# Optimization experiments

Hardware: AMD Instinct MI355X
Metric: run time of the kernel (lower is better)

## Reference

```python
import jax, jax.numpy as jnp
import numpy as np

KAPPA = 10000.0
B_CONST = 0.5


def pe_matrix(L, dim):
    # pe[j,i] = sin(j/kappa^(i/dim)) for even i, cos(j/kappa^((i-1)/dim)) for odd i
    j = jnp.arange(L, dtype=jnp.float32)[:, None]
    i = jnp.arange(dim, dtype=jnp.float32)[None, :]
    even = (jnp.arange(dim) % 2 == 0)[None, :]
    expo = jnp.where(even, i, i - 1.0) / dim
    ang = j / (KAPPA ** expo)
    return jnp.where(even, jnp.sin(ang), jnp.cos(ang))  # [L, dim]


def setup_inputs() -> dict:
    key = jax.random.key(0)
    ks = jax.random.split(key, 6)
    B, N, L, d, n = 4, 8, 1024, 256, 3
    theta = jax.random.normal(ks[0], (B, N, L, d), dtype=jnp.float32)
    xi = jax.random.normal(ks[1], (B, N, L, n), dtype=jnp.float32)
    edge_attr = jax.random.normal(ks[2], (B, L, N * (N - 1) * 2), dtype=jnp.float32)
    s = 1.0 / np.sqrt(d)
    Wq = jax.random.normal(ks[3], (d, d), dtype=jnp.float32) * s
    Wk = jax.random.normal(ks[4], (d, d), dtype=jnp.float32) * s
    Wv = jax.random.normal(ks[5], (d, d), dtype=jnp.float32) * s
    return {"theta": theta, "xi": xi, "edge_attr": edge_attr, "Wq": Wq, "Wk": Wk, "Wv": Wv}


def reference(theta, xi, edge_attr, Wq, Wk, Wv):
    B, N, L, d = theta.shape
    n = xi.shape[-1]
    # positional encoding (dropout in eval mode = identity)
    theta = theta + pe_matrix(L, d)
    xi = xi + pe_matrix(L, n)
    edge_attr = edge_attr + pe_matrix(L, N * (N - 1) * 2)[None]

    causal = jnp.triu(jnp.ones((L, L), dtype=bool), 1)  # True above diagonal
    neg_inf = jnp.float32(-jnp.inf)

    # feature path: standard causal scaled-dot-product attention
    q = jnp.einsum('bnld,ed->bnle', theta, Wq)
    k = jnp.einsum('bnld,ed->bnle', theta, Wk)
    v = jnp.einsum('bnld,ed->bnle', theta, Wv)
    scores = jnp.einsum('bnqd,bnkd->bnqk', q, k) / jnp.sqrt(jnp.float32(d))
    scores = jnp.where(causal, neg_inf, scores)
    h_out = jnp.einsum('bnqk,bnkd->bnqd', jax.nn.softmax(scores, axis=-1), v)

    # equivariant path: pairwise squared-distance attention
    D = xi[:, :, :, None, :] - xi[:, :, None, :, :]  # [B,N,L,L,n]
    sq = jnp.sum(D * D, axis=-1)                     # [B,N,L,L]
    sq = jnp.where(causal, neg_inf, sq)
    beta = jax.nn.softmax(sq, axis=-1)
    mbeta = beta * (1.0 - jnp.eye(L, dtype=beta.dtype))  # zero the diagonal
    second = B_CONST * jnp.einsum('bnqk,bnkc->bnqc', mbeta, xi)
    third = B_CONST * jnp.sum(mbeta, axis=-1, keepdims=True) * xi
    x_out = xi + second - third

    return h_out, x_out, edge_attr
```

## Files before the change

### kernel.cpp

```cpp
#include <hip/hip_runtime.h>
#include <math.h>

#define L    1024
#define D    256
#define NCH  3
#define HEADS 32
#define EDIM 112
#define BATCH 4

typedef __bf16 bf8_t __attribute__((ext_vector_type(8)));
typedef float  f4_t  __attribute__((ext_vector_type(4)));

typedef __attribute__((address_space(1))) const void GVC;
typedef __attribute__((address_space(3))) void LDSV;

__device__ inline unsigned short f2bf(float x) {
    unsigned u = __float_as_uint(x);
    u += 0x7FFFu + ((u >> 16) & 1u);
    return (unsigned short)(u >> 16);
}
__device__ inline float bf2f(unsigned short h) {
    return __uint_as_float(((unsigned)h) << 16);
}

__global__ void prep_kernel(const float* __restrict__ edge, const float* __restrict__ xi,
                            const float* __restrict__ Wq, const float* __restrict__ Wk,
                            const float* __restrict__ Wv,
                            float* __restrict__ pe_d, float* __restrict__ eout,
                            float* __restrict__ xsb, unsigned short* __restrict__ whb)
{
    int idx = blockIdx.x * blockDim.x + threadIdx.x;
    if (idx < L * D) {
        int l = idx >> 8, i = idx & (D - 1);
        float expo = (float)(i & ~1) * (1.0f / (float)D);
        float ang = (float)l * __powf(10000.0f, -expo);
        pe_d[idx] = (i & 1) ? cosf(ang) : sinf(ang);
    } else if (idx < L * D + BATCH * L * EDIM) {
        int j = idx - L * D;
        int i = j % EDIM;
        int l = (j / EDIM) % L;
        float expo = (float)(i & ~1) * (1.0f / (float)EDIM);
        float ang = (float)l * __powf(10000.0f, -expo);
        eout[j] = edge[j] + ((i & 1) ? cosf(ang) : sinf(ang));
    } else if (idx < L * D + BATCH * L * EDIM + HEADS * L * NCH) {
        int j = idx - (L * D + BATCH * L * EDIM);
        int c = j % 3;
        int l = (j / 3) & (L - 1);
        float ang = (c == 2) ? (float)l * 0.0021544347f : (float)l;
        float pe = (c == 1) ? cosf(ang) : sinf(ang);
        xsb[j] = xi[j] + pe;
    } else {
        int j = idx - (L * D + BATCH * L * EDIM + HEADS * L * NCH);
        if (j < 3 * 8192) {
            int wsel = j >> 13;
            int t = j & 8191;
            int g = t >> 9, u = (t >> 4) & 31, rr = t & 15;
            const float* W = (wsel == 0) ? Wq : (wsel == 1) ? Wk : Wv;
            const float4* s = reinterpret_cast<const float4*>(&W[(size_t)(g * 16 + rr) * D + u * 8]);
            float4 a = s[0], b = s[1];
            float x[8] = {a.x, a.y, a.z, a.w, b.x, b.y, b.z, b.w};
            union { unsigned short us[8]; float4 f4; } hv;
            #pragma unroll
            for (int q = 0; q < 8; q++) hv.us[q] = f2bf(x[q]);
            *reinterpret_cast<float4*>(&whb[(size_t)wsel * 65536 + g * 4096 + u * 128 + rr * 8]) = hv.f4;
        }
    }
}

__global__ __launch_bounds__(512) void qkv_mfma(
    const float* __restrict__ theta, const float* __restrict__ pe_d,
    const unsigned short* __restrict__ whb,
    unsigned short* __restrict__ qh, unsigned short* __restrict__ ql,
    unsigned short* __restrict__ kh, unsigned short* __restrict__ vt)
{
    __shared__ __align__(16) unsigned short XsH[2][4096];
    __shared__ __align__(16) unsigned short XsL[2][4096];
    __shared__ __align__(16) unsigned short Ws[2][8192];

    int tid = threadIdx.x;
    int w = tid >> 6, lane = tid & 63;
    int quad = lane >> 4, l16 = lane & 15;
    int eh = w & 1;
    int xq = w >> 1;

    int b = blockIdx.x;
    int xcd = b & 7, r = b >> 3;
    int wsel = r % 3;
    int panel = (r / 3) * 8 + xcd;
    int rowBase = panel * 128;
    const unsigned short* wsrc = whb + (size_t)wsel * 65536;

    int sr = tid >> 2;
    int ks8 = (tid & 3) * 8;
    int cg = sr >> 4, cr = sr & 15, cu = tid & 3;
    int xoff = cg * 512 + cu * 128 + cr * 8;

    const float* tp_base = &theta[(size_t)(rowBase + sr) * D + ks8];
    const float* pp_base = &pe_d[(size_t)((rowBase + sr) & (L - 1)) * D + ks8];

    f4_t acc[16];
    #pragma unroll
    for (int i = 0; i < 16; i++) acc[i] = (f4_t){0.f, 0.f, 0.f, 0.f};

    auto stageW = [&](int kt, int buf) {
        #pragma unroll
        for (int j = 0; j < 2; j++) {
            int g = w * 2 + j;
            __builtin_amdgcn_global_load_lds(
                (GVC*)(wsrc + (size_t)g * 4096 + kt * 512 + lane * 8),
                (LDSV*)(Ws[buf] + g * 512), 16, 0, 0);
        }
    };
    auto loadX = [&](int kt, float* xv) {
        const float* tp = tp_base + kt * 32;
        const float* pp = pp_base + kt * 32;
        float4 t0 = reinterpret_cast<const float4*>(tp)[0];
        float4 t1 = reinterpret_cast<const float4*>(tp)[1];
        float4 p0 = reinterpret_cast<const float4*>(pp)[0];
        float4 p1 = reinterpret_cast<const float4*>(pp)[1];
        xv[0] = t0.x + p0.x; xv[1] = t0.y + p0.y; xv[2] = t0.z + p0.z; xv[3] = t0.w + p0.w;
        xv[4] = t1.x + p1.x; xv[5] = t1.y + p1.y; xv[6] = t1.z + p1.z; xv[7] = t1.w + p1.w;
    };
    auto convX = [&](const float* xv, int buf) {
        union { unsigned short us[8]; float4 f4; } h, lo;
        #pragma unroll
        for (int e = 0; e < 8; e++) {
            unsigned short hh = f2bf(xv[e]);
            h.us[e] = hh;
            lo.us[e] = f2bf(xv[e] - bf2f(hh));
        }
        *reinterpret_cast<float4*>(&XsH[buf][xoff]) = h.f4;
        *reinterpret_cast<float4*>(&XsL[buf][xoff]) = lo.f4;
    };

    {
        float xv[8];
        loadX(0, xv);
        convX(xv, 0);
        stageW(0, 0);
    }
    __syncthreads();

    #define FR(buf2d, g16) (*reinterpret_cast<const bf8_t*>(&(buf2d)[(g16) * 512 + quad * 128 + l16 * 8]))

    for (int kt = 0; kt < 8; kt++) {
        int buf = kt & 1;

        float xn[8];
        if (kt < 7) {
            stageW(kt + 1, buf ^ 1);
            loadX(kt + 1, xn);
        }
        __builtin_amdgcn_sched_barrier(0);

        bf8_t bxh[2], bxl[2];
        #pragma unroll
        for (int nx = 0; nx < 2; nx++) {
            bxh[nx] = FR(XsH[buf], xq * 2 + nx);
            bxl[nx] = FR(XsL[buf], xq * 2 + nx);
        }

        if (wsel < 2) {
            #pragma unroll
            for (int ne = 0; ne < 8; ne++) {
                bf8_t aw = FR(Ws[buf], eh * 8 + ne);
                #pragma unroll
                for (int nx = 0; nx < 2; nx++) {
                    acc[ne * 2 + nx] = __builtin_amdgcn_mfma_f32_16x16x32_bf16(aw, bxh[nx], acc[ne * 2 + nx], 0, 0, 0);
                    acc[ne * 2 + nx] = __builtin_amdgcn_mfma_f32_16x16x32_bf16(aw, bxl[nx], acc[ne * 2 + nx], 0, 0, 0);
                }
            }
        } else {
            #pragma unroll
            for (int ne = 0; ne < 8; ne++) {
                bf8_t bw = FR(Ws[buf], eh * 8 + ne);
                #pragma unroll
                for (int mx = 0; mx < 2; mx++) {
                    acc[mx * 8 + ne] = __builtin_amdgcn_mfma_f32_16x16x32_bf16(bxh[mx], bw, acc[mx * 8 + ne], 0, 0, 0);
                    acc[mx * 8 + ne] = __builtin_amdgcn_mfma_f32_16x16x32_bf16(bxl[mx], bw, acc[mx * 8 + ne], 0, 0, 0);
                }
            }
        }

        if (kt < 7) convX(xn, buf ^ 1);
        __syncthreads();
    }
    #undef FR

    if (wsel < 2) {
        float scale = (wsel == 0) ? 0.0625f : 1.0f;
        #pragma unroll
        for (int ne = 0; ne < 8; ne++) {
            #pragma unroll
            for (int nx = 0; nx < 2; nx++) {
                int e0 = eh * 128 + ne * 16 + quad * 4;
                size_t row = rowBase + xq * 32 + nx * 16 + l16;
                union { unsigned short us[4]; unsigned long long u; } ph, pl;
                #pragma unroll
                for (int rr = 0; rr < 4; rr++) {
                    float x = acc[ne * 2 + nx][rr] * scale;
                    unsigned short h = f2bf(x);
                    ph.us[rr] = h;
                    pl.us[rr] = f2bf(x - bf2f(h));
                }
                if (wsel == 0) {
                    *reinterpret_cast<unsigned long long*>(&qh[row * D + e0]) = ph.u;
                    *reinterpret_cast<unsigned long long*>(&ql[row * D + e0]) = pl.u;
                } else {
                    int e0s = e0 ^ ((l16 & 7) << 3);
                    *reinterpret_cast<unsigned long long*>(&kh[row * D + e0s]) = ph.u;
                }
            }
        }
    } else {
        #pragma unroll
        for (int mx = 0; mx < 2; mx++) {
            #pragma unroll
            for (int ne = 0; ne < 8; ne++) {
                int row0 = rowBase + xq * 32 + mx * 16 + quad * 4;
                int e = eh * 128 + ne * 16 + l16;
                int head = row0 >> 10, kb = (row0 & 1023) >> 5, kk = row0 & 31;
                union { unsigned short us[4]; unsigned long long u; } pk;
                #pragma unroll
                for (int rr = 0; rr < 4; rr++) pk.us[rr] = f2bf(acc[mx * 8 + ne][rr]);
                int us_sw = (e * 32 + kk) ^ (((e >> 1) & 3) << 3);
                *reinterpret_cast<unsigned long long*>(
                    &vt[((size_t)(head * 32 + kb)) * 8192 + us_sw]) = pk.u;
            }
        }
    }
}

__device__ __forceinline__ void stage_tile(
    const unsigned short* kht, const unsigned short* vtt,
    unsigned short* Ks, unsigned short* Vs, int kt, int buf, int w, int lane)
{
    #pragma unroll
    for (int i = 0; i < 2; i++) {
        int ch = w * 2 + i;
        __builtin_amdgcn_global_load_lds(
            (GVC*)(kht + (size_t)kt * 8192 + ch * 512 + lane * 8),
            (LDSV*)(Ks + buf * 8192 + ch * 512), 16, 0, 0);
        __builtin_amdgcn_global_load_lds(
            (GVC*)(vtt + (size_t)kt * 8192 + ch * 512 + lane * 8),
            (LDSV*)(Vs + buf * 8192 + ch * 512), 16, 0, 0);
    }
}

__global__ __launch_bounds__(512) void attn_v7(
    const unsigned short* __restrict__ qh, const unsigned short* __restrict__ ql,
    const unsigned short* __restrict__ kh, const unsigned short* __restrict__ vt,
    float* __restrict__ hout)
{
    __shared__ __align__(16) unsigned short Ks[2 * 8192];
    __shared__ __align__(16) unsigned short Vs[2 * 8192];
    __shared__ __align__(16) unsigned short Pb[8][16 * 40];
    __shared__ unsigned short lds_pad[4200];

    int tid = threadIdx.x;
    int w = tid >> 6, lane = tid & 63;
    int quad = lane >> 4, l16 = lane & 15;
    int b = blockIdx.x;
    int head = ((b & 7) << 2) + (b >> 6);
    int s = (b >> 3) & 7;
    int u = (w < 4) ? (4 * s + w) : (63 - 4 * s - (w - 4));
    int Ts = 32 - 2 * s;
    int lim = u >> 1;
    size_t hb = (size_t)head * (L * D);
    const unsigned short* kht = kh + hb;
    const unsigned short* vtt = vt + (size_t)head * (32 * 8192);
    unsigned short* Pw = Pb[w];

    if (hout == nullptr) lds_pad[tid] = 1;

    int q_g = u * 16 + l16;

    f4_t qfh[8], qfl[8];
    {
        const unsigned short* ph = qh + hb + (size_t)q_g * D + quad * 8;
        const unsigned short* pl = ql + hb + (size_t)q_g * D + quad * 8;
        #pragma unroll
        for (int c = 0; c < 8; c++) {
            qfh[c] = *reinterpret_cast<const f4_t*>(ph + c * 32);
            qfl[c] = *reinterpret_cast<const f4_t*>(pl + c * 32);
        }
    }
    #pragma unroll
    for (int c = 0; c < 8; c++) {
        asm volatile("" : "+v"(qfh[c]));
        asm volatile("" : "+v"(qfl[c]));
    }

    stage_tile(kht, vtt, Ks, Vs, 0, 0, w, lane);

    f4_t acc[16];
    #pragma unroll
    for (int i = 0; i < 16; i++) acc[i] = (f4_t){0.f, 0.f, 0.f, 0.f};
    float mrun = -1e30f, lrun = 0.f;

    int xm = (l16 & 7) << 3;
    int vq = (quad * 8) ^ (((l16 >> 1) & 3) << 3);

    asm volatile("s_waitcnt vmcnt(0)" ::: "memory");
    __syncthreads();

    #pragma unroll 1
    for (int kt = 0; kt < Ts; kt++) {
        if (kt + 1 < Ts)
            stage_tile(kht, vtt, Ks, Vs, kt + 1, (kt + 1) & 1, w, lane);

        if (kt <= lim) {
            const unsigned short* Kb = Ks + (kt & 1) * 8192;
            const unsigned short* Vb = Vs + (kt & 1) * 8192;
            int kBase = kt * 32;

            bf8_t kf0[8], kf1[8];
            #pragma unroll
            for (int c = 0; c < 8; c++) {
                int col = (quad * 8 + c * 32) ^ xm;
                kf0[c] = *reinterpret_cast<const bf8_t*>(&Kb[l16 * 256 + col]);
                kf1[c] = *reinterpret_cast<const bf8_t*>(&Kb[(16 + l16) * 256 + col]);
            }
            const unsigned short* vpb = Vb + l16 * 32 + vq;
            bf8_t vfA[8];
            #pragma unroll
            for (int dt = 0; dt < 8; dt++)
                vfA[dt] = *reinterpret_cast<const bf8_t*>(vpb + dt * 512);

            f4_t s0a = (f4_t){0.f,0.f,0.f,0.f}, s0b = (f4_t){0.f,0.f,0.f,0.f};
            f4_t s1a = (f4_t){0.f,0.f,0.f,0.f}, s1b = (f4_t){0.f,0.f,0.f,0.f};
            #pragma unroll
            for (int c = 0; c < 8; c += 2) {
                s0a = __builtin_amdgcn_mfma_f32_16x16x32_bf16(kf0[c],     __builtin_bit_cast(bf8_t, qfh[c]),     s0a, 0, 0, 0);
                s0b = __builtin_amdgcn_mfma_f32_16x16x32_bf16(kf0[c + 1], __builtin_bit_cast(bf8_t, qfh[c + 1]), s0b, 0, 0, 0);
                s0a = __builtin_amdgcn_mfma_f32_16x16x32_bf16(kf0[c],     __builtin_bit_cast(bf8_t, qfl[c]),     s0a, 0, 0, 0);
                s0b = __builtin_amdgcn_mfma_f32_16x16x32_bf16(kf0[c + 1], __builtin_bit_cast(bf8_t, qfl[c + 1]), s0b, 0, 0, 0);
            }
            #pragma unroll
            for (int c = 0; c < 8; c += 2) {
                s1a = __builtin_amdgcn_mfma_f32_16x16x32_bf16(kf1[c],     __builtin_bit_cast(bf8_t, qfh[c]),     s1a, 0, 0, 0);
                s1b = __builtin_amdgcn_mfma_f32_16x16x32_bf16(kf1[c + 1], __builtin_bit_cast(bf8_t, qfh[c + 1]), s1b, 0, 0, 0);
                s1a = __builtin_amdgcn_mfma_f32_16x16x32_bf16(kf1[c],     __builtin_bit_cast(bf8_t, qfl[c]),     s1a, 0, 0, 0);
                s1b = __builtin_amdgcn_mfma_f32_16x16x32_bf16(kf1[c + 1], __builtin_bit_cast(bf8_t, qfl[c + 1]), s1b, 0, 0, 0);
            }
            f4_t sc[2];
            sc[0] = s0a + s0b;
            sc[1] = s1a + s1b;

            float pv[2][4];
            float tm = -1e30f;
            #pragma unroll
            for (int t = 0; t < 2; t++)
                #pragma unroll
                for (int rr = 0; rr < 4; rr++) {
                    int key = kBase + t * 16 + quad * 4 + rr;
                    float sv = (key <= q_g) ? sc[t][rr] : -1e30f;
                    sc[t][rr] = sv;
                    tm = fmaxf(tm, sv);
                }
            tm = fmaxf(tm, __shfl_xor(tm, 16));
            tm = fmaxf(tm, __shfl_xor(tm, 32));
            bool grow = __any(tm > mrun);
            float mnew = fmaxf(mrun, tm);
            float alpha = grow ? __expf(mrun - mnew) : 1.0f;
            mrun = mnew;
            float ts = 0.f;
            #pragma unroll
            for (int t = 0; t < 2; t++)
                #pragma unroll
                for (int rr = 0; rr < 4; rr++) {
                    float p = __expf(sc[t][rr] - mnew);
                    pv[t][rr] = p;
                    ts += p;
                }
            ts += __shfl_xor(ts, 16);
            ts += __shfl_xor(ts, 32);
            lrun = lrun * alpha + ts;

            #pragma unroll
            for (int t = 0; t < 2; t++) {
                union { unsigned short us[4]; unsigned long long uu; } pk;
                #pragma unroll
                for (int rr = 0; rr < 4; rr++) pk.us[rr] = f2bf(pv[t][rr]);
                *reinterpret_cast<unsigned long long*>(&Pw[l16 * 40 + t * 16 + quad * 4]) = pk.uu;
            }
            bf8_t vfB[8];
            #pragma unroll
            for (int dt = 0; dt < 8; dt++)
                vfB[dt] = *reinterpret_cast<const bf8_t*>(vpb + (8 + dt) * 512);
            if (grow) {
                #pragma unroll
                for (int dt = 0; dt < 16; dt++) acc[dt] *= alpha;
            }
            asm volatile("s_waitcnt lgkmcnt(0)" ::: "memory");
            bf8_t pf = *reinterpret_cast<const bf8_t*>(&Pw[l16 * 40 + quad * 8]);
            #pragma unroll
            for (int dt = 0; dt < 8; dt++)
                acc[dt] = __builtin_amdgcn_mfma_f32_16x16x32_bf16(vfA[dt], pf, acc[dt], 0, 0, 0);
            #pragma unroll
            for (int dt = 0; dt < 8; dt++)
                acc[8 + dt] = __builtin_amdgcn_mfma_f32_16x16x32_bf16(vfB[dt], pf, acc[8 + dt], 0, 0, 0);
        }

        asm volatile("s_waitcnt vmcnt(0)" ::: "memory");
        __syncthreads();
    }

    float inv = 1.f / lrun;
    float* dst = hout + hb + (size_t)q_g * D + quad * 4;
    #pragma unroll
    for (int dt = 0; dt < 16; dt++) {
        float4 o = {acc[dt][0] * inv, acc[dt][1] * inv,
                    acc[dt][2] * inv, acc[dt][3] * inv};
        *reinterpret_cast<float4*>(dst + dt * 16) = o;
    }
}

__global__ __launch_bounds__(256) void equiv_kernel(
    const float* __restrict__ xsb, float* __restrict__ xout)
{
    __shared__ float xs[L * NCH];
    int head = blockIdx.y;
    int tid = threadIdx.x;
    const float4* src = reinterpret_cast<const float4*>(xsb + (size_t)head * L * NCH);
    #pragma unroll
    for (int it = 0; it < 3; it++)
        reinterpret_cast<float4*>(xs)[tid + it * 256] = src[tid + it * 256];
    __syncthreads();

    int w = tid >> 6, lane = tid & 63;
    int q = blockIdx.x * 4 + w;
    float xq0 = xs[q * 3 + 0], xq1 = xs[q * 3 + 1], xq2 = xs[q * 3 + 2];

    float m = 0.f;
    for (int k = lane; k < q; k += 64) {
        float d0 = xq0 - xs[k * 3 + 0];
        float d1 = xq1 - xs[k * 3 + 1];
        float d2 = xq2 - xs[k * 3 + 2];
        m = fmaxf(m, d0 * d0 + d1 * d1 + d2 * d2);
    }
    #pragma unroll
    for (int off = 1; off < 64; off <<= 1) m = fmaxf(m, __shfl_xor(m, off));

    float s0 = 0.f, s1 = 0.f, s2 = 0.f, sn = 0.f;
    for (int k = lane; k < q; k += 64) {
        float d0 = xq0 - xs[k * 3 + 0];
        float d1 = xq1 - xs[k * 3 + 1];
        float d2 = xq2 - xs[k * 3 + 2];
        float wgt = __expf(d0 * d0 + d1 * d1 + d2 * d2 - m);
        sn += wgt;
        s0 += wgt * xs[k * 3 + 0];
        s1 += wgt * xs[k * 3 + 1];
        s2 += wgt * xs[k * 3 + 2];
    }
    #pragma unroll
    for (int off = 1; off < 64; off <<= 1) {
        sn += __shfl_xor(sn, off);
        s0 += __shfl_xor(s0, off);
        s1 += __shfl_xor(s1, off);
        s2 += __shfl_xor(s2, off);
    }
    float Z = sn + __expf(-m);
    float inv = 0.5f / Z;
    if (lane == 0) {
        size_t ob = (size_t)head * L * NCH + (size_t)q * NCH;
        xout[ob + 0] = xq0 + inv * (s0 - sn * xq0);
        xout[ob + 1] = xq1 + inv * (s1 - sn * xq1);
        xout[ob + 2] = xq2 + inv * (s2 - sn * xq2);
    }
}

extern "C" void kernel_launch(void* const* d_in, const int* in_sizes, int n_in,
                              void* d_out, int out_size, void* d_ws, size_t ws_size,
                              hipStream_t stream)
{
    (void)in_sizes; (void)n_in; (void)out_size; (void)ws_size;
    const float* theta = (const float*)d_in[0];
    const float* xi    = (const float*)d_in[1];
    const float* edge  = (const float*)d_in[2];
    const float* Wq    = (const float*)d_in[3];
    const float* Wk    = (const float*)d_in[4];
    const float* Wv    = (const float*)d_in[5];

    float* out  = (float*)d_out;
    float* hout = out;
    float* xout = out + 8388608;
    float* eout = out + 8388608 + 98304;

    const size_t NE = 8388608;
    unsigned short* base = (unsigned short*)d_ws;
    unsigned short* qh  = base;
    unsigned short* ql  = base + NE;
    unsigned short* kh  = base + 2 * NE;
    unsigned short* vt  = base + 3 * NE;
    unsigned short* whb = base + 4 * NE;
    float* pe_d = (float*)(base + 4 * NE + 196608);
    float* xsb  = pe_d + L * D;

    prep_kernel<<<3296, 256, 0, stream>>>(edge, xi, Wq, Wk, Wv, pe_d, eout, xsb, whb);
    equiv_kernel<<<dim3(L / 4, HEADS), 256, 0, stream>>>(xsb, xout);
    qkv_mfma<<<768, 512, 0, stream>>>(theta, pe_d, whb, qh, ql, kh, vt);
    attn_v7<<<256, 512, 0, stream>>>(qh, ql, kh, vt, hout);
}
```

Baseline: 230.6 us.

## Deepen LDS pipelines to four stages and keep activations in registers

```diff
diff --git a/kernel.cpp b/kernel.cpp
--- a/kernel.cpp
+++ b/kernel.cpp
@@ -73,9 +73,7 @@
     unsigned short* __restrict__ qh, unsigned short* __restrict__ ql,
     unsigned short* __restrict__ kh, unsigned short* __restrict__ vt)
 {
-    __shared__ __align__(16) unsigned short XsH[2][4096];
-    __shared__ __align__(16) unsigned short XsL[2][4096];
-    __shared__ __align__(16) unsigned short Ws[2][8192];
+    __shared__ __align__(16) unsigned short Ws[4][8192];
 
     int tid = threadIdx.x;
     int w = tid >> 6, lane = tid & 63;
@@ -90,18 +88,6 @@
     int rowBase = panel * 128;
     const unsigned short* wsrc = whb + (size_t)wsel * 65536;
 
-    int sr = tid >> 2;
-    int ks8 = (tid & 3) * 8;
-    int cg = sr >> 4, cr = sr & 15, cu = tid & 3;
-    int xoff = cg * 512 + cu * 128 + cr * 8;
-
-    const float* tp_base = &theta[(size_t)(rowBase + sr) * D + ks8];
-    const float* pp_base = &pe_d[(size_t)((rowBase + sr) & (L - 1)) * D + ks8];
-
-    f4_t acc[16];
-    #pragma unroll
-    for (int i = 0; i < 16; i++) acc[i] = (f4_t){0.f, 0.f, 0.f, 0.f};
-
     auto stageW = [&](int kt, int buf) {
         #pragma unroll
         for (int j = 0; j < 2; j++) {
@@ -111,54 +97,58 @@
                 (LDSV*)(Ws[buf] + g * 512), 16, 0, 0);
         }
     };
-    auto loadX = [&](int kt, float* xv) {
-        const float* tp = tp_base + kt * 32;
-        const float* pp = pp_base + kt * 32;
-        float4 t0 = reinterpret_cast<const float4*>(tp)[0];
-        float4 t1 = reinterpret_cast<const float4*>(tp)[1];
-        float4 p0 = reinterpret_cast<const float4*>(pp)[0];
-        float4 p1 = reinterpret_cast<const float4*>(pp)[1];
-        xv[0] = t0.x + p0.x; xv[1] = t0.y + p0.y; xv[2] = t0.z + p0.z; xv[3] = t0.w + p0.w;
-        xv[4] = t1.x + p1.x; xv[5] = t1.y + p1.y; xv[6] = t1.z + p1.z; xv[7] = t1.w + p1.w;
-    };
-    auto convX = [&](const float* xv, int buf) {
-        union { unsigned short us[8]; float4 f4; } h, lo;
-        #pragma unroll
-        for (int e = 0; e < 8; e++) {
-            unsigned short hh = f2bf(xv[e]);
-            h.us[e] = hh;
-            lo.us[e] = f2bf(xv[e] - bf2f(hh));
-        }
-        *reinterpret_cast<float4*>(&XsH[buf][xoff]) = h.f4;
-        *reinterpret_cast<float4*>(&XsL[buf][xoff]) = lo.f4;
-    };
-
-    {
-        float xv[8];
-        loadX(0, xv);
-        convX(xv, 0);
-        stageW(0, 0);
-    }
-    __syncthreads();
+
+    stageW(0, 0);
+    stageW(1, 1);
+    stageW(2, 2);
+
+    f4_t xh[2][8], xl[2][8];
+    #pragma unroll
+    for (int nx = 0; nx < 2; nx++) {
+        int row = rowBase + xq * 32 + nx * 16 + l16;
+        const float* tp = &theta[(size_t)row * D + quad * 8];
+        const float* pp = &pe_d[(size_t)(row & (L - 1)) * D + quad * 8];
+        #pragma unroll
+        for (int kt = 0; kt < 8; kt++) {
+            float4 t0 = reinterpret_cast<const float4*>(tp + kt * 32)[0];
+            float4 t1 = reinterpret_cast<const float4*>(tp + kt * 32 + 4)[0];
+            float4 p0 = reinterpret_cast<const float4*>(pp + kt * 32)[0];
+            float4 p1 = reinterpret_cast<const float4*>(pp + kt * 32 + 4)[0];
+            float xv[8] = {t0.x + p0.x, t0.y + p0.y, t0.z + p0.z, t0.w + p0.w,
+                           t1.x + p1.x, t1.y + p1.y, t1.z + p1.z, t1.w + p1.w};
+            union { unsigned short us[8]; f4_t f; } hu, lu;
+            #pragma unroll
+            for (int e = 0; e < 8; e++) {
+                unsigned short hh = f2bf(xv[e]);
+                hu.us[e] = hh;
+                lu.us[e] = f2bf(xv[e] - bf2f(hh));
+            }
+            xh[nx][kt] = hu.f;
+            xl[nx][kt] = lu.f;
+        }
+    }
+    #pragma unroll
+    for (int nx = 0; nx < 2; nx++)
+        #pragma unroll
+        for (int kt = 0; kt < 8; kt++) {
+            asm volatile("" : "+v"(xh[nx][kt]));
+            asm volatile("" : "+v"(xl[nx][kt]));
+        }
+
+    f4_t acc[16];
+    #pragma unroll
+    for (int i = 0; i < 16; i++) acc[i] = (f4_t){0.f, 0.f, 0.f, 0.f};
 
     #define FR(buf2d, g16) (*reinterpret_cast<const bf8_t*>(&(buf2d)[(g16) * 512 + quad * 128 + l16 * 8]))
 
+    #pragma unroll
     for (int kt = 0; kt < 8; kt++) {
-        int buf = kt & 1;
-
-        float xn[8];
-        if (kt < 7) {
-            stageW(kt + 1, buf ^ 1);
-            loadX(kt + 1, xn);
-        }
+        int buf = kt & 3;
+        asm volatile("s_waitcnt vmcnt(4)" ::: "memory");
+        __builtin_amdgcn_s_barrier();
         __builtin_amdgcn_sched_barrier(0);
-
-        bf8_t bxh[2], bxl[2];
-        #pragma unroll
-        for (int nx = 0; nx < 2; nx++) {
-            bxh[nx] = FR(XsH[buf], xq * 2 + nx);
-            bxl[nx] = FR(XsL[buf], xq * 2 + nx);
-        }
+        int nt = (kt + 3 < 8) ? kt + 3 : 7;
+        stageW(nt, (kt + 3) & 3);
 
         if (wsel < 2) {
             #pragma unroll
@@ -166,8 +156,8 @@
                 bf8_t aw = FR(Ws[buf], eh * 8 + ne);
                 #pragma unroll
                 for (int nx = 0; nx < 2; nx++) {
-                    acc[ne * 2 + nx] = __builtin_amdgcn_mfma_f32_16x16x32_bf16(aw, bxh[nx], acc[ne * 2 + nx], 0, 0, 0);
-                    acc[ne * 2 + nx] = __builtin_amdgcn_mfma_f32_16x16x32_bf16(aw, bxl[nx], acc[ne * 2 + nx], 0, 0, 0);
+                    acc[ne * 2 + nx] = __builtin_amdgcn_mfma_f32_16x16x32_bf16(aw, __builtin_bit_cast(bf8_t, xh[nx][kt]), acc[ne * 2 + nx], 0, 0, 0);
+                    acc[ne * 2 + nx] = __builtin_amdgcn_mfma_f32_16x16x32_bf16(aw, __builtin_bit_cast(bf8_t, xl[nx][kt]), acc[ne * 2 + nx], 0, 0, 0);
                 }
             }
         } else {
@@ -176,14 +166,11 @@
                 bf8_t bw = FR(Ws[buf], eh * 8 + ne);
                 #pragma unroll
                 for (int mx = 0; mx < 2; mx++) {
-                    acc[mx * 8 + ne] = __builtin_amdgcn_mfma_f32_16x16x32_bf16(bxh[mx], bw, acc[mx * 8 + ne], 0, 0, 0);
-                    acc[mx * 8 + ne] = __builtin_amdgcn_mfma_f32_16x16x32_bf16(bxl[mx], bw, acc[mx * 8 + ne], 0, 0, 0);
-                }
-            }
-        }
-
-        if (kt < 7) convX(xn, buf ^ 1);
-        __syncthreads();
+                    acc[mx * 8 + ne] = __builtin_amdgcn_mfma_f32_16x16x32_bf16(__builtin_bit_cast(bf8_t, xh[mx][kt]), bw, acc[mx * 8 + ne], 0, 0, 0);
+                    acc[mx * 8 + ne] = __builtin_amdgcn_mfma_f32_16x16x32_bf16(__builtin_bit_cast(bf8_t, xl[mx][kt]), bw, acc[mx * 8 + ne], 0, 0, 0);
+                }
+            }
+        }
     }
     #undef FR
 
@@ -247,15 +234,14 @@
     }
 }
 
-__global__ __launch_bounds__(512) void attn_v7(
+__global__ __launch_bounds__(512) void attn_v9(
     const unsigned short* __restrict__ qh, const unsigned short* __restrict__ ql,
     const unsigned short* __restrict__ kh, const unsigned short* __restrict__ vt,
     float* __restrict__ hout)
 {
-    __shared__ __align__(16) unsigned short Ks[2 * 8192];
-    __shared__ __align__(16) unsigned short Vs[2 * 8192];
+    __shared__ __align__(16) unsigned short Ks[4 * 8192];
+    __shared__ __align__(16) unsigned short Vs[4 * 8192];
     __shared__ __align__(16) unsigned short Pb[8][16 * 40];
-    __shared__ unsigned short lds_pad[4200];
 
     int tid = threadIdx.x;
     int w = tid >> 6, lane = tid & 63;
@@ -271,8 +257,6 @@
     const unsigned short* vtt = vt + (size_t)head * (32 * 8192);
     unsigned short* Pw = Pb[w];
 
-    if (hout == nullptr) lds_pad[tid] = 1;
-
     int q_g = u * 16 + l16;
 
     f4_t qfh[8], qfl[8];
@@ -292,6 +276,8 @@
     }
 
     stage_tile(kht, vtt, Ks, Vs, 0, 0, w, lane);
+    stage_tile(kht, vtt, Ks, Vs, 1, 1, w, lane);
+    stage_tile(kht, vtt, Ks, Vs, 2, 2, w, lane);
 
     f4_t acc[16];
     #pragma unroll
@@ -301,17 +287,17 @@
     int xm = (l16 & 7) << 3;
     int vq = (quad * 8) ^ (((l16 >> 1) & 3) << 3);
 
-    asm volatile("s_waitcnt vmcnt(0)" ::: "memory");
-    __syncthreads();
-
     #pragma unroll 1
     for (int kt = 0; kt < Ts; kt++) {
-        if (kt + 1 < Ts)
-            stage_tile(kht, vtt, Ks, Vs, kt + 1, (kt + 1) & 1, w, lane);
+        asm volatile("s_waitcnt vmcnt(8)" ::: "memory");
+        __builtin_amdgcn_s_barrier();
+        __builtin_amdgcn_sched_barrier(0);
+        int nt = (kt + 3 < Ts) ? kt + 3 : Ts - 1;
+        stage_tile(kht, vtt, Ks, Vs, nt, (kt + 3) & 3, w, lane);
 
         if (kt <= lim) {
-            const unsigned short* Kb = Ks + (kt & 1) * 8192;
-            const unsigned short* Vb = Vs + (kt & 1) * 8192;
+            const unsigned short* Kb = Ks + (kt & 3) * 8192;
+            const unsigned short* Vb = Vs + (kt & 3) * 8192;
             int kBase = kt * 32;
 
             bf8_t kf0[8], kf1[8];
@@ -329,6 +315,7 @@
 
             f4_t s0a = (f4_t){0.f,0.f,0.f,0.f}, s0b = (f4_t){0.f,0.f,0.f,0.f};
             f4_t s1a = (f4_t){0.f,0.f,0.f,0.f}, s1b = (f4_t){0.f,0.f,0.f,0.f};
+            __builtin_amdgcn_s_setprio(1);
             #pragma unroll
             for (int c = 0; c < 8; c += 2) {
                 s0a = __builtin_amdgcn_mfma_f32_16x16x32_bf16(kf0[c],     __builtin_bit_cast(bf8_t, qfh[c]),     s0a, 0, 0, 0);
@@ -343,6 +330,7 @@
                 s1a = __builtin_amdgcn_mfma_f32_16x16x32_bf16(kf1[c],     __builtin_bit_cast(bf8_t, qfl[c]),     s1a, 0, 0, 0);
                 s1b = __builtin_amdgcn_mfma_f32_16x16x32_bf16(kf1[c + 1], __builtin_bit_cast(bf8_t, qfl[c + 1]), s1b, 0, 0, 0);
             }
+            __builtin_amdgcn_s_setprio(0);
             f4_t sc[2];
             sc[0] = s0a + s0b;
             sc[1] = s1a + s1b;
@@ -394,16 +382,15 @@
             }
             asm volatile("s_waitcnt lgkmcnt(0)" ::: "memory");
             bf8_t pf = *reinterpret_cast<const bf8_t*>(&Pw[l16 * 40 + quad * 8]);
+            __builtin_amdgcn_s_setprio(1);
             #pragma unroll
             for (int dt = 0; dt < 8; dt++)
                 acc[dt] = __builtin_amdgcn_mfma_f32_16x16x32_bf16(vfA[dt], pf, acc[dt], 0, 0, 0);
             #pragma unroll
             for (int dt = 0; dt < 8; dt++)
                 acc[8 + dt] = __builtin_amdgcn_mfma_f32_16x16x32_bf16(vfB[dt], pf, acc[8 + dt], 0, 0, 0);
-        }
-
-        asm volatile("s_waitcnt vmcnt(0)" ::: "memory");
-        __syncthreads();
+            __builtin_amdgcn_s_setprio(0);
+        }
     }
 
     float inv = 1.f / lrun;
@@ -500,5 +487,5 @@
     prep_kernel<<<3296, 256, 0, stream>>>(edge, xi, Wq, Wk, Wv, pe_d, eout, xsb, whb);
     equiv_kernel<<<dim3(L / 4, HEADS), 256, 0, stream>>>(xsb, xout);
     qkv_mfma<<<768, 512, 0, stream>>>(theta, pe_d, whb, qh, ql, kh, vt);
-    attn_v7<<<256, 512, 0, stream>>>(qh, ql, kh, vt, hout);
-}
+    attn_v9<<<256, 512, 0, stream>>>(qh, ql, kh, vt, hout);
+}
```

Measured after the change: 273.4 us. +18.5%, slower.

## Process two key tiles per barrier step in causal attention kernel

Applied to the files above, without the earlier changes.

```diff
diff --git a/kernel.cpp b/kernel.cpp
--- a/kernel.cpp
+++ b/kernel.cpp
@@ -231,31 +231,35 @@
     }
 }
 
-__device__ __forceinline__ void stage_tile(
+__device__ __forceinline__ void stage_super(
     const unsigned short* kht, const unsigned short* vtt,
-    unsigned short* Ks, unsigned short* Vs, int kt, int buf, int w, int lane)
+    unsigned short* Ks, unsigned short* Vs, int st, int buf, int w, int lane)
 {
     #pragma unroll
-    for (int i = 0; i < 2; i++) {
-        int ch = w * 2 + i;
-        __builtin_amdgcn_global_load_lds(
-            (GVC*)(kht + (size_t)kt * 8192 + ch * 512 + lane * 8),
-            (LDSV*)(Ks + buf * 8192 + ch * 512), 16, 0, 0);
-        __builtin_amdgcn_global_load_lds(
-            (GVC*)(vtt + (size_t)kt * 8192 + ch * 512 + lane * 8),
-            (LDSV*)(Vs + buf * 8192 + ch * 512), 16, 0, 0);
-    }
-}
-
-__global__ __launch_bounds__(512) void attn_v7(
+    for (int j = 0; j < 2; j++) {
+        int t = st * 2 + j;
+        #pragma unroll
+        for (int i = 0; i < 2; i++) {
+            int ch = w * 2 + i;
+            __builtin_amdgcn_global_load_lds(
+                (GVC*)(kht + (size_t)t * 8192 + ch * 512 + lane * 8),
+                (LDSV*)(Ks + buf * 16384 + j * 8192 + ch * 512), 16, 0, 0);
+            __builtin_amdgcn_global_load_lds(
+                (GVC*)(vtt + (size_t)t * 8192 + ch * 512 + lane * 8),
+                (LDSV*)(Vs + buf * 16384 + j * 8192 + ch * 512), 16, 0, 0);
+        }
+    }
+}
+
+__global__ __launch_bounds__(512) __attribute__((amdgpu_waves_per_eu(2, 2)))
+void attn_v10(
     const unsigned short* __restrict__ qh, const unsigned short* __restrict__ ql,
     const unsigned short* __restrict__ kh, const unsigned short* __restrict__ vt,
     float* __restrict__ hout)
 {
-    __shared__ __align__(16) unsigned short Ks[2 * 8192];
-    __shared__ __align__(16) unsigned short Vs[2 * 8192];
-    __shared__ __align__(16) unsigned short Pb[8][16 * 40];
-    __shared__ unsigned short lds_pad[4200];
+    __shared__ __align__(16) unsigned short Ks[2 * 16384];
+    __shared__ __align__(16) unsigned short Vs[2 * 16384];
+    __shared__ __align__(16) unsigned short Pb[8][2][16 * 40];
 
     int tid = threadIdx.x;
     int w = tid >> 6, lane = tid & 63;
@@ -265,13 +269,13 @@
     int s = (b >> 3) & 7;
     int u = (w < 4) ? (4 * s + w) : (63 - 4 * s - (w - 4));
     int Ts = 32 - 2 * s;
-    int lim = u >> 1;
+    int nSup = Ts >> 1;
+    int limS = u >> 2;
     size_t hb = (size_t)head * (L * D);
     const unsigned short* kht = kh + hb;
     const unsigned short* vtt = vt + (size_t)head * (32 * 8192);
-    unsigned short* Pw = Pb[w];
-
-    if (hout == nullptr) lds_pad[tid] = 1;
+    unsigned short* PwA = Pb[w][0];
+    unsigned short* PwB = Pb[w][1];
 
     int q_g = u * 16 + l16;
 
@@ -291,7 +295,7 @@
         asm volatile("" : "+v"(qfl[c]));
     }
 
-    stage_tile(kht, vtt, Ks, Vs, 0, 0, w, lane);
+    stage_super(kht, vtt, Ks, Vs, 0, 0, w, lane);
 
     f4_t acc[16];
     #pragma unroll
@@ -301,62 +305,93 @@
     int xm = (l16 & 7) << 3;
     int vq = (quad * 8) ^ (((l16 >> 1) & 3) << 3);
 
-    asm volatile("s_waitcnt vmcnt(0)" ::: "memory");
-    __syncthreads();
-
     #pragma unroll 1
-    for (int kt = 0; kt < Ts; kt++) {
-        if (kt + 1 < Ts)
-            stage_tile(kht, vtt, Ks, Vs, kt + 1, (kt + 1) & 1, w, lane);
-
-        if (kt <= lim) {
-            const unsigned short* Kb = Ks + (kt & 1) * 8192;
-            const unsigned short* Vb = Vs + (kt & 1) * 8192;
-            int kBase = kt * 32;
+    for (int st = 0; st < nSup; st++) {
+        asm volatile("s_waitcnt vmcnt(0)" ::: "memory");
+        __builtin_amdgcn_s_barrier();
+        __builtin_amdgcn_sched_barrier(0);
+        int ns = (st + 1 < nSup) ? st + 1 : nSup - 1;
+        stage_super(kht, vtt, Ks, Vs, ns, (st + 1) & 1, w, lane);
+
+        if (st <= limS) {
+            const unsigned short* Kb0 = Ks + (st & 1) * 16384;
+            const unsigned short* Vb0 = Vs + (st & 1) * 16384;
+            const unsigned short* Kb1 = Kb0 + 8192;
+            const unsigned short* Vb1 = Vb0 + 8192;
+            int kBase = st * 64;
 
             bf8_t kf0[8], kf1[8];
             #pragma unroll
             for (int c = 0; c < 8; c++) {
                 int col = (quad * 8 + c * 32) ^ xm;
-                kf0[c] = *reinterpret_cast<const bf8_t*>(&Kb[l16 * 256 + col]);
-                kf1[c] = *reinterpret_cast<const bf8_t*>(&Kb[(16 + l16) * 256 + col]);
-            }
-            const unsigned short* vpb = Vb + l16 * 32 + vq;
+                kf0[c] = *reinterpret_cast<const bf8_t*>(&Kb0[l16 * 256 + col]);
+                kf1[c] = *reinterpret_cast<const bf8_t*>(&Kb0[(16 + l16) * 256 + col]);
+            }
+            f4_t a0 = (f4_t){0.f,0.f,0.f,0.f}, a1 = (f4_t){0.f,0.f,0.f,0.f};
+            f4_t a2 = (f4_t){0.f,0.f,0.f,0.f}, a3 = (f4_t){0.f,0.f,0.f,0.f};
+            __builtin_amdgcn_s_setprio(1);
+            #pragma unroll
+            for (int c = 0; c < 8; c += 2) {
+                a0 = __builtin_amdgcn_mfma_f32_16x16x32_bf16(kf0[c],     __builtin_bit_cast(bf8_t, qfh[c]),     a0, 0, 0, 0);
+                a1 = __builtin_amdgcn_mfma_f32_16x16x32_bf16(kf0[c + 1], __builtin_bit_cast(bf8_t, qfh[c + 1]), a1, 0, 0, 0);
+                a0 = __builtin_amdgcn_mfma_f32_16x16x32_bf16(kf0[c],     __builtin_bit_cast(bf8_t, qfl[c]),     a0, 0, 0, 0);
+                a1 = __builtin_amdgcn_mfma_f32_16x16x32_bf16(kf0[c + 1], __builtin_bit_cast(bf8_t, qfl[c + 1]), a1, 0, 0, 0);
+                a2 = __builtin_amdgcn_mfma_f32_16x16x32_bf16(kf1[c],     __builtin_bit_cast(bf8_t, qfh[c]),     a2, 0, 0, 0);
+                a3 = __builtin_amdgcn_mfma_f32_16x16x32_bf16(kf1[c + 1], __builtin_bit_cast(bf8_t, qfh[c + 1]), a3, 0, 0, 0);
+                a2 = __builtin_amdgcn_mfma_f32_16x16x32_bf16(kf1[c],     __builtin_bit_cast(bf8_t, qfl[c]),     a2, 0, 0, 0);
+                a3 = __builtin_amdgcn_mfma_f32_16x16x32_bf16(kf1[c + 1], __builtin_bit_cast(bf8_t, qfl[c + 1]), a3, 0, 0, 0);
+            }
+            __builtin_amdgcn_s_setprio(0);
+            f4_t scA[2];
+            scA[0] = a0 + a1;
+            scA[1] = a2 + a3;
+
+            bf8_t kf2[8], kf3[8];
+            #pragma unroll
+            for (int c = 0; c < 8; c++) {
+                int col = (quad * 8 + c * 32) ^ xm;
+                kf2[c] = *reinterpret_cast<const bf8_t*>(&Kb1[l16 * 256 + col]);
+                kf3[c] = *reinterpret_cast<const bf8_t*>(&Kb1[(16 + l16) * 256 + col]);
+            }
+            f4_t b0 = (f4_t){0.f,0.f,0.f,0.f}, b1 = (f4_t){0.f,0.f,0.f,0.f};
+            f4_t b2 = (f4_t){0.f,0.f,0.f,0.f}, b3 = (f4_t){0.f,0.f,0.f,0.f};
+            __builtin_amdgcn_s_setprio(1);
+            #pragma unroll
+            for (int c = 0; c < 8; c += 2) {
+                b0 = __builtin_amdgcn_mfma_f32_16x16x32_bf16(kf2[c],     __builtin_bit_cast(bf8_t, qfh[c]),     b0, 0, 0, 0);
+                b1 = __builtin_amdgcn_mfma_f32_16x16x32_bf16(kf2[c + 1], __builtin_bit_cast(bf8_t, qfh[c + 1]), b1, 0, 0, 0);
+                b0 = __builtin_amdgcn_mfma_f32_16x16x32_bf16(kf2[c],     __builtin_bit_cast(bf8_t, qfl[c]),     b0, 0, 0, 0);
+                b1 = __builtin_amdgcn_mfma_f32_16x16x32_bf16(kf2[c + 1], __builtin_bit_cast(bf8_t, qfl[c + 1]), b1, 0, 0, 0);
+                b2 = __builtin_amdgcn_mfma_f32_16x16x32_bf16(kf3[c],     __builtin_bit_cast(bf8_t, qfh[c]),     b2, 0, 0, 0);
+                b3 = __builtin_amdgcn_mfma_f32_16x16x32_bf16(kf3[c + 1], __builtin_bit_cast(bf8_t, qfh[c + 1]), b3, 0, 0, 0);
+                b2 = __builtin_amdgcn_mfma_f32_16x16x32_bf16(kf3[c],     __builtin_bit_cast(bf8_t, qfl[c]),     b2, 0, 0, 0);
+                b3 = __builtin_amdgcn_mfma_f32_16x16x32_bf16(kf3[c + 1], __builtin_bit_cast(bf8_t, qfl[c + 1]), b3, 0, 0, 0);
+            }
+            __builtin_amdgcn_s_setprio(0);
+            f4_t scB[2];
+            scB[0] = b0 + b1;
+            scB[1] = b2 + b3;
+
+            const unsigned short* vp0 = Vb0 + l16 * 32 + vq;
+            const unsigned short* vp1 = Vb1 + l16 * 32 + vq;
             bf8_t vfA[8];
             #pragma unroll
             for (int dt = 0; dt < 8; dt++)
-                vfA[dt] = *reinterpret_cast<const bf8_t*>(vpb + dt * 512);
-
-            f4_t s0a = (f4_t){0.f,0.f,0.f,0.f}, s0b = (f4_t){0.f,0.f,0.f,0.f};
-            f4_t s1a = (f4_t){0.f,0.f,0.f,0.f}, s1b = (f4_t){0.f,0.f,0.f,0.f};
-            #pragma unroll
-            for (int c = 0; c < 8; c += 2) {
-                s0a = __builtin_amdgcn_mfma_f32_16x16x32_bf16(kf0[c],     __builtin_bit_cast(bf8_t, qfh[c]),     s0a, 0, 0, 0);
-                s0b = __builtin_amdgcn_mfma_f32_16x16x32_bf16(kf0[c + 1], __builtin_bit_cast(bf8_t, qfh[c + 1]), s0b, 0, 0, 0);
-                s0a = __builtin_amdgcn_mfma_f32_16x16x32_bf16(kf0[c],     __builtin_bit_cast(bf8_t, qfl[c]),     s0a, 0, 0, 0);
-                s0b = __builtin_amdgcn_mfma_f32_16x16x32_bf16(kf0[c + 1], __builtin_bit_cast(bf8_t, qfl[c + 1]), s0b, 0, 0, 0);
-            }
-            #pragma unroll
-            for (int c = 0; c < 8; c += 2) {
-                s1a = __builtin_amdgcn_mfma_f32_16x16x32_bf16(kf1[c],     __builtin_bit_cast(bf8_t, qfh[c]),     s1a, 0, 0, 0);
-                s1b = __builtin_amdgcn_mfma_f32_16x16x32_bf16(kf1[c + 1], __builtin_bit_cast(bf8_t, qfh[c + 1]), s1b, 0, 0, 0);
-                s1a = __builtin_amdgcn_mfma_f32_16x16x32_bf16(kf1[c],     __builtin_bit_cast(bf8_t, qfl[c]),     s1a, 0, 0, 0);
-                s1b = __builtin_amdgcn_mfma_f32_16x16x32_bf16(kf1[c + 1], __builtin_bit_cast(bf8_t, qfl[c + 1]), s1b, 0, 0, 0);
-            }
-            f4_t sc[2];
-            sc[0] = s0a + s0b;
-            sc[1] = s1a + s1b;
-
-            float pv[2][4];
+                vfA[dt] = *reinterpret_cast<const bf8_t*>(vp0 + dt * 512);
+
+            float pvA[2][4], pvB[2][4];
             float tm = -1e30f;
             #pragma unroll
             for (int t = 0; t < 2; t++)
                 #pragma unroll
                 for (int rr = 0; rr < 4; rr++) {
-                    int key = kBase + t * 16 + quad * 4 + rr;
-                    float sv = (key <= q_g) ? sc[t][rr] : -1e30f;
-                    sc[t][rr] = sv;
-                    tm = fmaxf(tm, sv);
+                    int keyA = kBase + t * 16 + quad * 4 + rr;
+                    int keyB = keyA + 32;
+                    float svA = (keyA <= q_g) ? scA[t][rr] : -1e30f;
+                    float svB = (keyB <= q_g) ? scB[t][rr] : -1e30f;
+                    scA[t][rr] = svA;
+                    scB[t][rr] = svB;
+                    tm = fmaxf(tm, fmaxf(svA, svB));
                 }
             tm = fmaxf(tm, __shfl_xor(tm, 16));
             tm = fmaxf(tm, __shfl_xor(tm, 32));
@@ -369,9 +404,11 @@
             for (int t = 0; t < 2; t++)
                 #pragma unroll
                 for (int rr = 0; rr < 4; rr++) {
-                    float p = __expf(sc[t][rr] - mnew);
-                    pv[t][rr] = p;
-                    ts += p;
+                    float pA = __expf(scA[t][rr] - mnew);
+                    float pB = __expf(scB[t][rr] - mnew);
+                    pvA[t][rr] = pA;
+                    pvB[t][rr] = pB;
+                    ts += pA + pB;
                 }
             ts += __shfl_xor(ts, 16);
             ts += __shfl_xor(ts, 32);
@@ -379,31 +416,55 @@
 
             #pragma unroll
             for (int t = 0; t < 2; t++) {
-                union { unsigned short us[4]; unsigned long long uu; } pk;
-                #pragma unroll
-                for (int rr = 0; rr < 4; rr++) pk.us[rr] = f2bf(pv[t][rr]);
-                *reinterpret_cast<unsigned long long*>(&Pw[l16 * 40 + t * 16 + quad * 4]) = pk.uu;
-            }
+                union { unsigned short us[4]; unsigned long long uu; } pkA, pkB;
+                #pragma unroll
+                for (int rr = 0; rr < 4; rr++) {
+                    pkA.us[rr] = f2bf(pvA[t][rr]);
+                    pkB.us[rr] = f2bf(pvB[t][rr]);
+                }
+                *reinterpret_cast<unsigned long long*>(&PwA[l16 * 40 + t * 16 + quad * 4]) = pkA.uu;
+                *reinterpret_cast<unsigned long long*>(&PwB[l16 * 40 + t * 16 + quad * 4]) = pkB.uu;
+            }
+            if (grow) {
+                #pragma unroll
+                for (int dt = 0; dt < 16; dt++) acc[dt] *= alpha;
+            }
+            asm volatile("s_waitcnt lgkmcnt(0)" ::: "memory");
+            bf8_t pfA = *reinterpret_cast<const bf8_t*>(&PwA[l16 * 40 + quad * 8]);
+            __builtin_amdgcn_s_setprio(1);
+            #pragma unroll
+            for (int dt = 0; dt < 8; dt++)
+                acc[dt] = __builtin_amdgcn_mfma_f32_16x16x32_bf16(vfA[dt], pfA, acc[dt], 0, 0, 0);
+            __builtin_amdgcn_s_setprio(0);
+            bf8_t vfA2[8];
+            #pragma unroll
+            for (int dt = 0; dt < 8; dt++)
+                vfA2[dt] = *reinterpret_cast<const bf8_t*>(vp0 + (8 + dt) * 512);
+            __builtin_amdgcn_s_setprio(1);
+            #pragma unroll
+            for (int dt = 0; dt < 8; dt++)
+                acc[8 + dt] = __builtin_amdgcn_mfma_f32_16x16x32_bf16(vfA2[dt], pfA, acc[8 + dt], 0, 0, 0);
+            __builtin_amdgcn_s_setprio(0);
             bf8_t vfB[8];
             #pragma unroll
             for (int dt = 0; dt < 8; dt++)
-                vfB[dt] = *reinterpret_cast<const bf8_t*>(vpb + (8 + dt) * 512);
-            if (grow) {
-                #pragma unroll
-                for (int dt = 0; dt < 16; dt++) acc[dt] *= alpha;
-            }
-            asm volatile("s_waitcnt lgkmcnt(0)" ::: "memory");
-            bf8_t pf = *reinterpret_cast<const bf8_t*>(&Pw[l16 * 40 + quad * 8]);
-            #pragma unroll
-            for (int dt = 0; dt < 8; dt++)
-                acc[dt] = __builtin_amdgcn_mfma_f32_16x16x32_bf16(vfA[dt], pf, acc[dt], 0, 0, 0);
-            #pragma unroll
-            for (int dt = 0; dt < 8; dt++)
-                acc[8 + dt] = __builtin_amdgcn_mfma_f32_16x16x32_bf16(vfB[dt], pf, acc[8 + dt], 0, 0, 0);
-        }
-
-        asm volatile("s_waitcnt vmcnt(0)" ::: "memory");
-        __syncthreads();
+                vfB[dt] = *reinterpret_cast<const bf8_t*>(vp1 + dt * 512);
+            bf8_t pfB = *reinterpret_cast<const bf8_t*>(&PwB[l16 * 40 + quad * 8]);
+            __builtin_amdgcn_s_setprio(1);
+            #pragma unroll
+            for (int dt = 0; dt < 8; dt++)
+                acc[dt] = __builtin_amdgcn_mfma_f32_16x16x32_bf16(vfB[dt], pfB, acc[dt], 0, 0, 0);
+            __builtin_amdgcn_s_setprio(0);
+            bf8_t vfB2[8];
+            #pragma unroll
+            for (int dt = 0; dt < 8; dt++)
+                vfB2[dt] = *reinterpret_cast<const bf8_t*>(vp1 + (8 + dt) * 512);
+            __builtin_amdgcn_s_setprio(1);
+            #pragma unroll
+            for (int dt = 0; dt < 8; dt++)
+                acc[8 + dt] = __builtin_amdgcn_mfma_f32_16x16x32_bf16(vfB2[dt], pfB, acc[8 + dt], 0, 0, 0);
+            __builtin_amdgcn_s_setprio(0);
+        }
     }
 
     float inv = 1.f / lrun;
@@ -500,5 +561,5 @@
     prep_kernel<<<3296, 256, 0, stream>>>(edge, xi, Wq, Wk, Wv, pe_d, eout, xsb, whb);
     equiv_kernel<<<dim3(L / 4, HEADS), 256, 0, stream>>>(xsb, xout);
     qkv_mfma<<<768, 512, 0, stream>>>(theta, pe_d, whb, qh, ql, kh, vt);
-    attn_v7<<<256, 512, 0, stream>>>(qh, ql, kh, vt, hout);
-}
+    attn_v10<<<256, 512, 0, stream>>>(qh, ql, kh, vt, hout);
+}
```

Result: faster. 221.1 us (-4.1%).
